# Kernel tuning notes

Measured on AMD Instinct MI355X. Metric: run time of the kernel, lower is better.

## Reference

```python
import jax, jax.numpy as jnp
import numpy as np

B, N, M = 8192, 4096, 256


def setup_inputs() -> dict:
    key = jax.random.key(0)
    k_x, k_keep, k_w1, k_b1, k_w2, k_b2 = jax.random.split(key, 6)
    x = jax.random.normal(k_x, (B, N), dtype=jnp.float32)
    keep = jax.random.uniform(k_keep, (B, N)) < 0.5
    x = jnp.where(keep, x, 0.0)
    # Linear params, PyTorch-style fan-in scaling
    W1 = jax.random.normal(k_w1, (N, M), dtype=jnp.float32) / np.sqrt(N)
    b1 = jax.random.normal(k_b1, (M,), dtype=jnp.float32) * 0.01
    W2 = jax.random.normal(k_w2, (M, N), dtype=jnp.float32) / np.sqrt(M)
    b2 = jax.random.normal(k_b2, (N,), dtype=jnp.float32) * 0.01
    return {"x": x, "W1": W1, "b1": b1, "W2": W2, "b2": b2}


def reference(x, W1, b1, W2, b2):
    # f2(relu(f1(x)))
    f = jax.nn.relu(x @ W1 + b1) @ W2 + b2  # [B, N]
    mask = x != 0
    # per-row sum over masked positions (vectorized version of the Python loop)
    s = jnp.sum(jnp.where(mask, f, 0.0), axis=1, keepdims=True)  # [B, 1]
    # rows with empty mask stay all-zero; guard divide-by-zero for those rows
    s_safe = jnp.where(s == 0.0, 1.0, s)
    y = jnp.where(mask, f / s_safe, 0.0)
    return y
```

## Files before the change

### kernel.cpp

```cpp
#include <hip/hip_runtime.h>

typedef _Float16 f16;
typedef _Float16 f16x8 __attribute__((ext_vector_type(8)));
typedef float f32x4 __attribute__((ext_vector_type(4)));

#define MFMA16(a,b,c) __builtin_amdgcn_mfma_f32_16x16x32_f16((a),(b),(c),0,0,0)

__device__ __forceinline__ void gload16(const void* g, void* l) {
  __builtin_amdgcn_global_load_lds(
      (const __attribute__((address_space(1))) void*)g,
      (__attribute__((address_space(3))) void*)l, 16, 0, 0);
}

__device__ __forceinline__ int swz(int r, int c) {
  return r * 32 + ((c ^ (r & 3)) << 3);
}

__device__ __forceinline__ void split8n(const f32x4 v0, const f32x4 v1,
                                        f16x8& hv, f16x8& lv) {
#pragma unroll
  for (int j = 0; j < 4; ++j) {
    f16 h0 = (f16)v0[j]; hv[j] = h0; lv[j] = (f16)(v0[j] - (float)h0);
    f16 h1 = (f16)v1[j]; hv[j + 4] = h1; lv[j + 4] = (f16)(v1[j] - (float)h1);
  }
}

__global__ __launch_bounds__(256) void k_prep(const float* __restrict__ in,
                                              f16* __restrict__ oh, f16* __restrict__ ol,
                                              int R, int C, int trShift) {
  __shared__ float t[64][65];
  int c0 = blockIdx.x * 64, r0 = blockIdx.y * 64;
  int tid = threadIdx.x;
#pragma unroll
  for (int i = 0; i < 16; ++i) {
    int idx = tid + i * 256;
    int r = idx >> 6, c = idx & 63;
    t[r][c] = in[(size_t)(r0 + r) * C + (c0 + c)];
  }
  __syncthreads();
  int ktiles = R >> 5;
  int TRm1 = (1 << trShift) - 1;
#pragma unroll
  for (int w = 0; w < 2; ++w) {
    int idx = tid + w * 256;
    int nn = idx >> 3, cc8 = idx & 7;
    f32x4 v0, v1;
#pragma unroll
    for (int j = 0; j < 4; ++j) v0[j] = t[cc8 * 8 + j][nn];
#pragma unroll
    for (int j = 0; j < 4; ++j) v1[j] = t[cc8 * 8 + 4 + j][nn];
    f16x8 hv, lv;
    split8n(v0, v1, hv, lv);
    int gn = c0 + nn, gk = r0 + cc8 * 8;
    size_t tileIdx = (size_t)(gn >> trShift) * ktiles + (gk >> 5);
    size_t off = (tileIdx << (trShift + 5)) + ((size_t)(gn & TRm1) << 5) +
                 (((cc8 & 3) ^ (gn & 3)) << 3);
    *(f16x8*)&oh[off] = hv;
    *(f16x8*)&ol[off] = lv;
  }
}

__global__ __launch_bounds__(256, 3) void k_g1(
    const float* __restrict__ X, const f16* __restrict__ Bht,
    const f16* __restrict__ Blt, unsigned char* __restrict__ mb,
    float* __restrict__ partials) {
  __shared__ f16 smB[3][8192];
  int bx = blockIdx.x, nb = blockIdx.y, kc = blockIdx.z;
  int tid = threadIdx.x;
  int wv = tid >> 6, ln = tid & 63, lr = ln & 15, lg = ln >> 4;
  const int NS = 32;
  int m0 = bx * 128, kb0 = kc * 1024;
  size_t bt0 = ((size_t)nb * 128 + (size_t)kc * 32) * 4096;
  bool domask = (nb == 0);

  const float* xb = X + (size_t)(m0 + wv * 32 + lr) * 4096 + kb0 + lg * 8;
  const size_t XF = (size_t)16 * 4096;

  f32x4 areg[4];
  f16x8 ah[2], al[2];
  f32x4 acc[2][8] = {};

  auto issueA = [&](int s) {
#pragma unroll
    for (int fi = 0; fi < 2; ++fi) {
      const float* p = xb + (size_t)fi * XF + s * 32;
      areg[fi * 2] = *(const f32x4*)p;
      areg[fi * 2 + 1] = *(const f32x4*)(p + 4);
    }
  };
  auto stageB = [&](int s, int buf) {
    const f16* bh = Bht + bt0 + (size_t)s * 4096;
    const f16* bl = Blt + bt0 + (size_t)s * 4096;
#pragma unroll
    for (int i = 0; i < 2; ++i)
      gload16(bh + ((i * 4 + wv) * 512 + ln * 8), &smB[buf][(i * 4 + wv) * 512]);
#pragma unroll
    for (int i = 0; i < 2; ++i)
      gload16(bl + ((i * 4 + wv) * 512 + ln * 8),
              &smB[buf][4096 + (i * 4 + wv) * 512]);
  };
  auto splitA = [&](int s) {
#pragma unroll
    for (int fi = 0; fi < 2; ++fi)
      split8n(areg[fi * 2], areg[fi * 2 + 1], ah[fi], al[fi]);
    if (domask) {
#pragma unroll
      for (int fi = 0; fi < 2; ++fi) {
        unsigned m = 0;
#pragma unroll
        for (int j = 0; j < 4; ++j) {
          if (areg[fi * 2][j] != 0.f) m |= 1u << j;
          if (areg[fi * 2 + 1][j] != 0.f) m |= 1u << (4 + j);
        }
        int row = m0 + wv * 32 + fi * 16 + lr;
        int gk = kb0 + s * 32 + lg * 8;
        mb[(size_t)row * 512 + (gk >> 3)] = (unsigned char)m;
      }
    }
  };

  issueA(0);
  stageB(0, 0);
  stageB(1, 1);
  asm volatile("s_waitcnt vmcnt(4)" ::: "memory");
  __builtin_amdgcn_sched_barrier(0);
  splitA(0);
  __builtin_amdgcn_s_barrier();

  int cb = 0;
  for (int s = 0; s < NS; ++s) {
    bool moreA = (s + 1) < NS;
    bool moreB = (s + 2) < NS;
    if (moreA) issueA(s + 1);
    if (moreB) {
      int pb = cb + 2; if (pb >= 3) pb -= 3;
      stageB(s + 2, pb);
    }
#pragma unroll
    for (int g = 0; g < 2; ++g) {
      f16x8 fbh[4], fbl[4];
#pragma unroll
      for (int j = 0; j < 4; ++j) {
        int c = (g * 4 + j) * 16 + lr;
        fbh[j] = *(const f16x8*)&smB[cb][swz(c, lg)];
        fbl[j] = *(const f16x8*)&smB[cb][4096 + swz(c, lg)];
      }
#pragma unroll
      for (int fi = 0; fi < 2; ++fi)
#pragma unroll
        for (int j = 0; j < 4; ++j) {
          acc[fi][g * 4 + j] = MFMA16(ah[fi], fbh[j], acc[fi][g * 4 + j]);
          acc[fi][g * 4 + j] = MFMA16(ah[fi], fbl[j], acc[fi][g * 4 + j]);
          acc[fi][g * 4 + j] = MFMA16(al[fi], fbh[j], acc[fi][g * 4 + j]);
        }
    }
    if (moreA) {
      if (moreB)
        asm volatile("s_waitcnt vmcnt(4)" ::: "memory");
      else
        asm volatile("s_waitcnt vmcnt(0)" ::: "memory");
      __builtin_amdgcn_sched_barrier(0);
      splitA(s + 1);
      __builtin_amdgcn_s_barrier();
    }
    cb = cb + 1; if (cb >= 3) cb -= 3;
  }

  float* pout = partials + (size_t)kc * 8192 * 256;
#pragma unroll
  for (int fi = 0; fi < 2; ++fi)
#pragma unroll
    for (int fj = 0; fj < 8; ++fj)
#pragma unroll
      for (int q = 0; q < 4; ++q) {
        int row = m0 + wv * 32 + fi * 16 + lg * 4 + q;
        int col = nb * 128 + fj * 16 + lr;
        pout[(size_t)row * 256 + col] = acc[fi][fj][q];
      }
}

__global__ __launch_bounds__(256) void k_hsplit(const float* __restrict__ p,
                                                const float* __restrict__ b1,
                                                f16* __restrict__ Hh,
                                                f16* __restrict__ Hl) {
  int g = blockIdx.x * 256 + threadIdx.x;
  int r = g >> 5, c = g & 31;
  const size_t CH = (size_t)8192 * 256;
  const float* p0 = p + (size_t)r * 256 + c * 8;
  f32x4 s0 = *(const f32x4*)p0, s1 = *(const f32x4*)(p0 + 4);
#pragma unroll
  for (int q = 1; q < 4; ++q) {
    f32x4 d0 = *(const f32x4*)(p0 + q * CH), d1 = *(const f32x4*)(p0 + q * CH + 4);
#pragma unroll
    for (int j = 0; j < 4; ++j) { s0[j] += d0[j]; s1[j] += d1[j]; }
  }
  f32x4 bb0 = *(const f32x4*)(b1 + c * 8), bb1 = *(const f32x4*)(b1 + c * 8 + 4);
  f32x4 v0, v1;
#pragma unroll
  for (int j = 0; j < 4; ++j) {
    float v = s0[j] + bb0[j];
    v0[j] = v > 0.f ? v : 0.f;
    float w = s1[j] + bb1[j];
    v1[j] = w > 0.f ? w : 0.f;
  }
  f16x8 hv, lv;
  split8n(v0, v1, hv, lv);
  size_t tileIdx = (size_t)(r >> 7) * 8 + (c >> 2);
  size_t off = tileIdx * 4096 + ((size_t)(r & 127) << 5) + (((c & 3) ^ (r & 3)) << 3);
  *(f16x8*)&Hh[off] = hv;
  *(f16x8*)&Hl[off] = lv;
}

__global__ __launch_bounds__(256, 2) void k_gemm2b(
    const f16* __restrict__ At_h, const f16* __restrict__ At_l,
    const f16* __restrict__ Bt_h, const f16* __restrict__ Bt_l,
    const float* __restrict__ b2, const unsigned* __restrict__ maskw,
    f16* __restrict__ fout, float* __restrict__ partials) {
  __shared__ f16 smA[2][2][4096];
  __shared__ f16 smB[2][2][4096];
  __shared__ unsigned mlds[128][4];
  __shared__ float rsum[128][2];
  int bx = blockIdx.x, by = blockIdx.y;
  int m0 = bx * 128, n0 = by * 128;
  int tid = threadIdx.x;
  int wv = tid >> 6, ln = tid & 63, lr = ln & 15, lg = ln >> 4;
  int wr = wv >> 1, wc = wv & 1;
#pragma unroll
  for (int i = 0; i < 2; ++i) {
    int idx = tid + i * 256;
    mlds[idx >> 2][idx & 3] =
        maskw[(size_t)(m0 + (idx >> 2)) * 128 + by * 4 + (idx & 3)];
  }
  size_t at0 = (size_t)bx * 8 * 4096;
  size_t bt0 = (size_t)by * 8 * 4096;

  auto stage = [&](int s, int buf) {
#pragma unroll
    for (int w = 0; w < 2; ++w) {
      size_t o = (size_t)(w * 4 + wv) * 512 + (size_t)ln * 8;
      gload16(At_h + at0 + (size_t)s * 4096 + o, &smA[buf][0][(w * 4 + wv) * 512]);
      gload16(At_l + at0 + (size_t)s * 4096 + o, &smA[buf][1][(w * 4 + wv) * 512]);
      gload16(Bt_h + bt0 + (size_t)s * 4096 + o, &smB[buf][0][(w * 4 + wv) * 512]);
      gload16(Bt_l + bt0 + (size_t)s * 4096 + o, &smB[buf][1][(w * 4 + wv) * 512]);
    }
  };

  f32x4 acc[4][4] = {};
  stage(0, 0);
  __syncthreads();
  int cur = 0;
  for (int s = 0; s < 8; ++s) {
    if (s + 1 < 8) stage(s + 1, cur ^ 1);
    f16x8 fah[4], fal[4], fbh[4], fbl[4];
#pragma unroll
    for (int f = 0; f < 4; ++f) {
      int r = wr * 64 + f * 16 + lr;
      fah[f] = *(const f16x8*)&smA[cur][0][swz(r, lg)];
      fal[f] = *(const f16x8*)&smA[cur][1][swz(r, lg)];
      int c = wc * 64 + f * 16 + lr;
      fbh[f] = *(const f16x8*)&smB[cur][0][swz(c, lg)];
      fbl[f] = *(const f16x8*)&smB[cur][1][swz(c, lg)];
    }
#pragma unroll
    for (int fi = 0; fi < 4; ++fi)
#pragma unroll
      for (int fj = 0; fj < 4; ++fj) {
        acc[fi][fj] = MFMA16(fah[fi], fbh[fj], acc[fi][fj]);
        acc[fi][fj] = MFMA16(fah[fi], fbl[fj], acc[fi][fj]);
        acc[fi][fj] = MFMA16(fal[fi], fbh[fj], acc[fi][fj]);
      }
    __syncthreads();
    cur ^= 1;
  }

  float rp[4][4] = {};
#pragma unroll
  for (int fi = 0; fi < 4; ++fi)
#pragma unroll
    for (int fj = 0; fj < 4; ++fj)
#pragma unroll
      for (int q = 0; q < 4; ++q) {
        int row = wr * 64 + fi * 16 + lg * 4 + q;
        int col = wc * 64 + fj * 16 + lr;
        float v = acc[fi][fj][q] + b2[n0 + col];
        unsigned wd = mlds[row][col >> 5];
        float mv = ((wd >> (col & 31)) & 1u) ? v : 0.f;
        fout[(size_t)(m0 + row) * 4096 + (n0 + col)] = (f16)mv;
        rp[fi][q] += mv;
      }
#pragma unroll
  for (int fi = 0; fi < 4; ++fi)
#pragma unroll
    for (int q = 0; q < 4; ++q) {
      float sv = rp[fi][q];
      sv += __shfl_xor(sv, 1);
      sv += __shfl_xor(sv, 2);
      sv += __shfl_xor(sv, 4);
      sv += __shfl_xor(sv, 8);
      if (lr == 0) rsum[wr * 64 + fi * 16 + lg * 4 + q][wc] = sv;
    }
  __syncthreads();
  if (tid < 128)
    partials[(size_t)(m0 + tid) * 32 + by] = rsum[tid][0] + rsum[tid][1];
}

__global__ __launch_bounds__(256) void k_rowinv(const float* __restrict__ partials,
                                                float* __restrict__ inv) {
  int r = blockIdx.x * 256 + threadIdx.x;
  if (r < 8192) {
    float s = 0.f;
#pragma unroll 4
    for (int i = 0; i < 32; ++i) s += partials[(size_t)r * 32 + i];
    float ss = (s == 0.f) ? 1.f : s;
    inv[r] = 1.f / ss;
  }
}

__global__ __launch_bounds__(256) void k_scale16(const f16* __restrict__ f,
                                                 const float* __restrict__ inv,
                                                 float* __restrict__ out) {
  int v = blockIdx.x * 256 + threadIdx.x;
  float iv = inv[v >> 9];
  f16x8 d = *(const f16x8*)(f + (size_t)v * 8);
  f32x4 o0, o1;
#pragma unroll
  for (int j = 0; j < 4; ++j) {
    o0[j] = (float)d[j] * iv;
    o1[j] = (float)d[4 + j] * iv;
  }
  *(f32x4*)(out + (size_t)v * 8) = o0;
  *(f32x4*)(out + (size_t)v * 8 + 4) = o1;
}

extern "C" void kernel_launch(void* const* d_in, const int* in_sizes, int n_in,
                              void* d_out, int out_size, void* d_ws, size_t ws_size,
                              hipStream_t stream) {
  const float* x  = (const float*)d_in[0];
  const float* W1 = (const float*)d_in[1];
  const float* b1 = (const float*)d_in[2];
  const float* W2 = (const float*)d_in[3];
  const float* b2 = (const float*)d_in[4];
  float* out = (float*)d_out;
  char* ws = (char*)d_ws;

  const size_t MB = (size_t)1 << 20;
  f16* W1t_h = (f16*)(ws + 0 * MB);
  f16* W1t_l = (f16*)(ws + 2 * MB);
  f16* W2t_h = (f16*)(ws + 4 * MB);
  f16* W2t_l = (f16*)(ws + 6 * MB);
  f16* Hh    = (f16*)(ws + 8 * MB);
  f16* Hl    = (f16*)(ws + 12 * MB);
  unsigned char* mb = (unsigned char*)(ws + 16 * MB);
  float* part1 = (float*)(ws + 20 * MB);
  float* part2 = (float*)(ws + 52 * MB);
  float* inv_s = (float*)(ws + 53 * MB);
  f16* fbuf    = (f16*)(ws + 54 * MB);

  k_prep<<<dim3(4, 64), 256, 0, stream>>>(W1, W1t_h, W1t_l, 4096, 256, 7);
  k_prep<<<dim3(64, 4), 256, 0, stream>>>(W2, W2t_h, W2t_l, 256, 4096, 7);
  k_g1<<<dim3(64, 2, 4), 256, 0, stream>>>(x, W1t_h, W1t_l, mb, part1);
  k_hsplit<<<1024, 256, 0, stream>>>(part1, b1, Hh, Hl);
  k_gemm2b<<<dim3(64, 32), 256, 0, stream>>>(Hh, Hl, W2t_h, W2t_l, b2,
                                             (const unsigned*)mb, fbuf, part2);
  k_rowinv<<<32, 256, 0, stream>>>(part2, inv_s);
  k_scale16<<<16384, 256, 0, stream>>>(fbuf, inv_s, out);
}
```

Baseline: 198.3 us.

## Enlarge second GEMM tile to 256x256 with 512-thread blocks

The second GEMM moves from 128x128 tiles with 256 threads to 256x256 tiles with 512 threads (8 waves, each computing 64x128). The H and W2 layouts and their prep and split kernels change to match the 256-row tiles, and the row-partial count drops from 32 to 16. The goal is more operand reuse from LDS, less global and L2 traffic per FLOP, and fewer partials to reduce. In exchange the kernel uses double the LDS and more accumulator registers, runs one block per CU, and launches only 512 blocks, which may leave the machine less occupied.

```diff
diff --git a/kernel.cpp b/kernel.cpp
--- a/kernel.cpp
+++ b/kernel.cpp
@@ -205,70 +205,77 @@
   }
   f16x8 hv, lv;
   split8n(v0, v1, hv, lv);
-  size_t tileIdx = (size_t)(r >> 7) * 8 + (c >> 2);
-  size_t off = tileIdx * 4096 + ((size_t)(r & 127) << 5) + (((c & 3) ^ (r & 3)) << 3);
+  size_t tileIdx = (size_t)(r >> 8) * 8 + (c >> 2);
+  size_t off = tileIdx * 8192 + ((size_t)(r & 255) << 5) + (((c & 3) ^ (r & 3)) << 3);
   *(f16x8*)&Hh[off] = hv;
   *(f16x8*)&Hl[off] = lv;
 }
 
-__global__ __launch_bounds__(256, 2) void k_gemm2b(
+__global__ __launch_bounds__(512, 1) void k_gemm2c(
     const f16* __restrict__ At_h, const f16* __restrict__ At_l,
     const f16* __restrict__ Bt_h, const f16* __restrict__ Bt_l,
     const float* __restrict__ b2, const unsigned* __restrict__ maskw,
     f16* __restrict__ fout, float* __restrict__ partials) {
-  __shared__ f16 smA[2][2][4096];
-  __shared__ f16 smB[2][2][4096];
-  __shared__ unsigned mlds[128][4];
-  __shared__ float rsum[128][2];
+  __shared__ f16 smA[2][2][8192];
+  __shared__ f16 smB[2][2][8192];
+  __shared__ unsigned mlds[256][8];
+  __shared__ float rsum[256][2];
   int bx = blockIdx.x, by = blockIdx.y;
-  int m0 = bx * 128, n0 = by * 128;
+  int m0 = bx * 256, n0 = by * 256;
   int tid = threadIdx.x;
-  int wv = tid >> 6, ln = tid & 63, lr = ln & 15, lg = ln >> 4;
-  int wr = wv >> 1, wc = wv & 1;
-#pragma unroll
-  for (int i = 0; i < 2; ++i) {
-    int idx = tid + i * 256;
-    mlds[idx >> 2][idx & 3] =
-        maskw[(size_t)(m0 + (idx >> 2)) * 128 + by * 4 + (idx & 3)];
-  }
-  size_t at0 = (size_t)bx * 8 * 4096;
-  size_t bt0 = (size_t)by * 8 * 4096;
+  int wid = tid >> 6, ln = tid & 63, lr = ln & 15, lg = ln >> 4;
+  int wr = wid >> 1, wc = wid & 1;
+#pragma unroll
+  for (int i = 0; i < 4; ++i) {
+    int idx = tid + i * 512;
+    mlds[idx >> 3][idx & 7] =
+        maskw[(size_t)(m0 + (idx >> 3)) * 128 + by * 8 + (idx & 7)];
+  }
+  size_t at0 = (size_t)bx * 8 * 8192;
+  size_t bt0 = (size_t)by * 8 * 8192;
 
   auto stage = [&](int s, int buf) {
 #pragma unroll
-    for (int w = 0; w < 2; ++w) {
-      size_t o = (size_t)(w * 4 + wv) * 512 + (size_t)ln * 8;
-      gload16(At_h + at0 + (size_t)s * 4096 + o, &smA[buf][0][(w * 4 + wv) * 512]);
-      gload16(At_l + at0 + (size_t)s * 4096 + o, &smA[buf][1][(w * 4 + wv) * 512]);
-      gload16(Bt_h + bt0 + (size_t)s * 4096 + o, &smB[buf][0][(w * 4 + wv) * 512]);
-      gload16(Bt_l + bt0 + (size_t)s * 4096 + o, &smB[buf][1][(w * 4 + wv) * 512]);
+    for (int i = 0; i < 2; ++i) {
+      size_t o = (size_t)(i * 8 + wid) * 512 + (size_t)ln * 8;
+      gload16(At_h + at0 + (size_t)s * 8192 + o, &smA[buf][0][(i * 8 + wid) * 512]);
+      gload16(At_l + at0 + (size_t)s * 8192 + o, &smA[buf][1][(i * 8 + wid) * 512]);
+      gload16(Bt_h + bt0 + (size_t)s * 8192 + o, &smB[buf][0][(i * 8 + wid) * 512]);
+      gload16(Bt_l + bt0 + (size_t)s * 8192 + o, &smB[buf][1][(i * 8 + wid) * 512]);
     }
   };
 
-  f32x4 acc[4][4] = {};
+  f32x4 acc[4][8] = {};
   stage(0, 0);
   __syncthreads();
   int cur = 0;
   for (int s = 0; s < 8; ++s) {
     if (s + 1 < 8) stage(s + 1, cur ^ 1);
-    f16x8 fah[4], fal[4], fbh[4], fbl[4];
+    f16x8 fah[4], fal[4];
 #pragma unroll
     for (int f = 0; f < 4; ++f) {
       int r = wr * 64 + f * 16 + lr;
       fah[f] = *(const f16x8*)&smA[cur][0][swz(r, lg)];
       fal[f] = *(const f16x8*)&smA[cur][1][swz(r, lg)];
-      int c = wc * 64 + f * 16 + lr;
-      fbh[f] = *(const f16x8*)&smB[cur][0][swz(c, lg)];
-      fbl[f] = *(const f16x8*)&smB[cur][1][swz(c, lg)];
-    }
-#pragma unroll
-    for (int fi = 0; fi < 4; ++fi)
-#pragma unroll
-      for (int fj = 0; fj < 4; ++fj) {
-        acc[fi][fj] = MFMA16(fah[fi], fbh[fj], acc[fi][fj]);
-        acc[fi][fj] = MFMA16(fah[fi], fbl[fj], acc[fi][fj]);
-        acc[fi][fj] = MFMA16(fal[fi], fbh[fj], acc[fi][fj]);
-      }
+    }
+#pragma unroll
+    for (int g = 0; g < 2; ++g) {
+      f16x8 fbh[4], fbl[4];
+#pragma unroll
+      for (int j = 0; j < 4; ++j) {
+        int c = wc * 128 + (g * 4 + j) * 16 + lr;
+        fbh[j] = *(const f16x8*)&smB[cur][0][swz(c, lg)];
+        fbl[j] = *(const f16x8*)&smB[cur][1][swz(c, lg)];
+      }
+#pragma unroll
+      for (int fi = 0; fi < 4; ++fi)
+#pragma unroll
+        for (int j = 0; j < 4; ++j) {
+          acc[fi][g * 4 + j] = MFMA16(fah[fi], fbh[j], acc[fi][g * 4 + j]);
+          acc[fi][g * 4 + j] = MFMA16(fah[fi], fbl[j], acc[fi][g * 4 + j]);
+          acc[fi][g * 4 + j] = MFMA16(fal[fi], fbh[j], acc[fi][g * 4 + j]);
+        }
+    }
     __syncthreads();
     cur ^= 1;
   }
@@ -277,11 +284,11 @@
 #pragma unroll
   for (int fi = 0; fi < 4; ++fi)
 #pragma unroll
-    for (int fj = 0; fj < 4; ++fj)
+    for (int fj = 0; fj < 8; ++fj)
 #pragma unroll
       for (int q = 0; q < 4; ++q) {
         int row = wr * 64 + fi * 16 + lg * 4 + q;
-        int col = wc * 64 + fj * 16 + lr;
+        int col = wc * 128 + fj * 16 + lr;
         float v = acc[fi][fj][q] + b2[n0 + col];
         unsigned wd = mlds[row][col >> 5];
         float mv = ((wd >> (col & 31)) & 1u) ? v : 0.f;
@@ -300,8 +307,8 @@
       if (lr == 0) rsum[wr * 64 + fi * 16 + lg * 4 + q][wc] = sv;
     }
   __syncthreads();
-  if (tid < 128)
-    partials[(size_t)(m0 + tid) * 32 + by] = rsum[tid][0] + rsum[tid][1];
+  if (tid < 256)
+    partials[(size_t)(m0 + tid) * 16 + by] = rsum[tid][0] + rsum[tid][1];
 }
 
 __global__ __launch_bounds__(256) void k_rowinv(const float* __restrict__ partials,
@@ -310,7 +317,7 @@
   if (r < 8192) {
     float s = 0.f;
 #pragma unroll 4
-    for (int i = 0; i < 32; ++i) s += partials[(size_t)r * 32 + i];
+    for (int i = 0; i < 16; ++i) s += partials[(size_t)r * 16 + i];
     float ss = (s == 0.f) ? 1.f : s;
     inv[r] = 1.f / ss;
   }
@@ -357,10 +364,10 @@
   f16* fbuf    = (f16*)(ws + 54 * MB);
 
   k_prep<<<dim3(4, 64), 256, 0, stream>>>(W1, W1t_h, W1t_l, 4096, 256, 7);
-  k_prep<<<dim3(64, 4), 256, 0, stream>>>(W2, W2t_h, W2t_l, 256, 4096, 7);
+  k_prep<<<dim3(64, 4), 256, 0, stream>>>(W2, W2t_h, W2t_l, 256, 4096, 8);
   k_g1<<<dim3(64, 2, 4), 256, 0, stream>>>(x, W1t_h, W1t_l, mb, part1);
   k_hsplit<<<1024, 256, 0, stream>>>(part1, b1, Hh, Hl);
-  k_gemm2b<<<dim3(64, 32), 256, 0, stream>>>(Hh, Hl, W2t_h, W2t_l, b2,
+  k_gemm2c<<<dim3(32, 16), 512, 0, stream>>>(Hh, Hl, W2t_h, W2t_l, b2,
                                              (const unsigned*)mb, fbuf, part2);
   k_rowinv<<<32, 256, 0, stream>>>(part2, inv_s);
   k_scale16<<<16384, 256, 0, stream>>>(fbuf, inv_s, out);
```

New measurement: 191.0 us. 3.7% less time.
